# Optimization experiments

Hardware: AMD Instinct MI355X
Metric: run time of the kernel (lower is better)

Reference implementation:

```python
import jax, jax.numpy as jnp
import numpy as np

N_NODES = 100000


def _gcn_norm(edge_index, num_nodes):
    # add self-loops, compute symmetric normalization D^-1/2 (A+I) D^-1/2
    loop = jnp.arange(num_nodes, dtype=edge_index.dtype)
    src = jnp.concatenate([edge_index[0], loop])
    dst = jnp.concatenate([edge_index[1], loop])
    deg = jax.ops.segment_sum(jnp.ones_like(src, dtype=jnp.float32), dst,
                              num_segments=num_nodes)
    dis = jnp.where(deg > 0, jax.lax.rsqrt(jnp.maximum(deg, 1.0)), 0.0)
    norm = dis[src] * dis[dst]  # [E+N]
    return src, dst, norm


def _gcn_conv(x, src, dst, norm, W, b, num_nodes):
    h = x @ W                               # [N, C_out]
    msg = h[src] * norm[:, None]            # gather + scale, [E+N, C_out]
    out = jax.ops.segment_sum(msg, dst, num_segments=num_nodes)
    return out + b


def setup_inputs() -> dict:
    key = jax.random.key(0)
    ks = jax.random.split(key, 8)
    N, E, D = N_NODES, 1600000, 128
    x = jax.random.normal(ks[0], (N, D), dtype=jnp.float32)
    edge_index = jax.random.randint(ks[1], (2, E), 0, N, dtype=jnp.int32)
    s = 1.0 / np.sqrt(D)
    W1 = jax.random.normal(ks[2], (D, D), dtype=jnp.float32) * s
    W2 = jax.random.normal(ks[3], (D, D), dtype=jnp.float32) * s
    W3 = jax.random.normal(ks[4], (D, D), dtype=jnp.float32) * s
    b1 = jnp.zeros((D,), jnp.float32)
    b2 = jnp.zeros((D,), jnp.float32)
    b3 = jnp.zeros((D,), jnp.float32)
    return {"x": x, "edge_index": edge_index, "W1": W1, "b1": b1,
            "W2": W2, "b2": b2, "W3": W3, "b3": b3}


def reference(x, edge_index, W1, b1, W2, b2, W3, b3):
    N = x.shape[0]
    src, dst, norm = _gcn_norm(edge_index, N)
    # layer 1 + relu (dropout p=0 / eval -> identity)
    x = jax.nn.relu(_gcn_conv(x, src, dst, norm, W1, b1, N))
    # layer 2 + relu
    x = jax.nn.relu(_gcn_conv(x, src, dst, norm, W2, b2, N))
    # final layer, no activation
    x = _gcn_conv(x, src, dst, norm, W3, b3, N)
    return x
```

## Files before the change

### kernel.cpp

```cpp
#include <hip/hip_runtime.h>

#define D 128
#define CAP 48
#define PSHIFT 8
#define PNODES 256
#define PMAX 512
#define CAPP 6144
#define EPB 8192

typedef unsigned short u16;
typedef __bf16 bf16_t;
typedef bf16_t bf16x8 __attribute__((ext_vector_type(8)));
typedef float f32x4v __attribute__((ext_vector_type(4)));


__device__ __forceinline__ u16 f2bf(float f) {
    unsigned u = __float_as_uint(f);
    return (u16)((u + 0x7FFFu + ((u >> 16) & 1u)) >> 16);
}

__device__ __forceinline__ float bf2f(u16 h) {
    return __uint_as_float((unsigned)h << 16);
}

__device__ __forceinline__ float4 bf2f4(ushort4 h) {
    float4 f;
    f.x = bf2f(h.x); f.y = bf2f(h.y); f.z = bf2f(h.z); f.w = bf2f(h.w);
    return f;
}

__device__ __forceinline__ void fma4(float4& acc, float xs, const float4& wv) {
    acc.x = fmaf(xs, wv.x, acc.x);
    acc.y = fmaf(xs, wv.y, acc.y);
    acc.z = fmaf(xs, wv.z, acc.z);
    acc.w = fmaf(xs, wv.w, acc.w);
}


__global__ __launch_bounds__(1024) void k_part(const int* __restrict__ src,
                                               const int* __restrict__ dstv,
                                               int* __restrict__ pcur,
                                               int* __restrict__ plist, int E, int P) {
    __shared__ int hist_l[PMAX];
    __shared__ int base_l[PMAX];
    int e0 = blockIdx.x * EPB;
    int e1 = min(e0 + EPB, E);

    for (int i = threadIdx.x; i < P; i += 1024) hist_l[i] = 0;
    __syncthreads();

    for (int e = e0 + threadIdx.x; e < e1; e += 1024)
        atomicAdd(&hist_l[dstv[e] >> PSHIFT], 1);
    __syncthreads();

    for (int i = threadIdx.x; i < P; i += 1024)
        base_l[i] = atomicAdd(&pcur[i], hist_l[i]);
    __syncthreads();

    for (int e = e0 + threadIdx.x; e < e1; e += 1024) {
        int s = src[e], d = dstv[e];
        int p = d >> PSHIFT;
        int pos = atomicAdd(&base_l[p], 1);
        if (pos < CAPP)
            plist[(size_t)p * CAPP + pos] = (s << PSHIFT) | (d & (PNODES - 1));
    }
}


__global__ __launch_bounds__(256) void k_build2(const int* __restrict__ plist,
                                                const int* __restrict__ pcur,
                                                int* __restrict__ cnt,
                                                int* __restrict__ slots, int N) {
    __shared__ int cnt_l[PNODES];
    __shared__ int slots_l[PNODES * CAP];
    int p = blockIdx.x;
    int node0 = p << PSHIFT;
    int nnodes = min(PNODES, N - node0);

    for (int t = threadIdx.x; t < PNODES; t += 256) cnt_l[t] = 0;
    __syncthreads();

    int nE = min(pcur[p], CAPP);
    for (int i = threadIdx.x; i < nE; i += 256) {
        int v = plist[(size_t)p * CAPP + i];
        int ln = v & (PNODES - 1);
        int s = (unsigned)v >> PSHIFT;
        int q = atomicAdd(&cnt_l[ln], 1);
        if (q < CAP) slots_l[ln * CAP + q] = s;
    }
    __syncthreads();

    for (int t = threadIdx.x; t < nnodes; t += 256) cnt[node0 + t] = cnt_l[t];
    int tot = nnodes * CAP;
    int* gs = slots + (size_t)node0 * CAP;
    for (int i = threadIdx.x; i < tot; i += 256) gs[i] = slots_l[i];
}

__global__ void k_dis(const int* __restrict__ cnt, float* __restrict__ dis, int N) {
    int i = blockIdx.x * 256 + threadIdx.x;
    if (i < N) dis[i] = rsqrtf((float)(cnt[i] + 1));
}


__global__ __launch_bounds__(256) void k_gemm(const float* __restrict__ X,
                                              const float* __restrict__ Wg,
                                              u16* __restrict__ H, int nchunks, int N) {
    __shared__ bf16_t sHi[D * D];
    __shared__ bf16_t sLo[D * D];

    for (int i = threadIdx.x; i < D * D; i += 256) {
        int k = i >> 7, n = i & 127;
        float w = Wg[i];
        bf16_t hi = (bf16_t)w;
        bf16_t lo = (bf16_t)(w - (float)hi);
        int idx = (n * D + k) ^ ((n & 7) << 3);
        sHi[idx] = hi;
        sLo[idx] = lo;
    }
    __syncthreads();

    int wv = threadIdx.x >> 6;
    int l  = threadIdx.x & 63;
    int lm = l & 15;
    int g  = l >> 4;

    for (int chunk = blockIdx.x; chunk < nchunks; chunk += gridDim.x) {
        int rowbase = chunk * 128 + wv * 32;
        if (rowbase >= N) continue;

        f32x4v acc[2][8];
#pragma unroll
        for (int rt = 0; rt < 2; ++rt)
#pragma unroll
            for (int c = 0; c < 8; ++c)
#pragma unroll
                for (int r = 0; r < 4; ++r) acc[rt][c][r] = 0.f;

#pragma unroll
        for (int t = 0; t < 4; ++t) {
            bf16x8 ahi[2], alo[2];
#pragma unroll
            for (int rt = 0; rt < 2; ++rt) {
                int row = rowbase + rt * 16 + lm;
                int rc = row < N ? row : N - 1;
                const float4* xp = (const float4*)(X + (size_t)rc * D + t * 32 + g * 8);
                float4 f0 = xp[0];
                float4 f1 = xp[1];
                float fv[8] = {f0.x, f0.y, f0.z, f0.w, f1.x, f1.y, f1.z, f1.w};
#pragma unroll
                for (int i = 0; i < 8; ++i) {
                    bf16_t hb = (bf16_t)fv[i];
                    ahi[rt][i] = hb;
                    alo[rt][i] = (bf16_t)(fv[i] - (float)hb);
                }
            }
#pragma unroll
            for (int c = 0; c < 8; ++c) {
                int idx = ((c * 16 + lm) * D + t * 32 + g * 8) ^ ((lm & 7) << 3);
                bf16x8 bhi = *(const bf16x8*)&sHi[idx];
                bf16x8 blo = *(const bf16x8*)&sLo[idx];
                acc[0][c] = __builtin_amdgcn_mfma_f32_16x16x32_bf16(ahi[0], bhi, acc[0][c], 0, 0, 0);
                acc[0][c] = __builtin_amdgcn_mfma_f32_16x16x32_bf16(ahi[0], blo, acc[0][c], 0, 0, 0);
                acc[0][c] = __builtin_amdgcn_mfma_f32_16x16x32_bf16(alo[0], bhi, acc[0][c], 0, 0, 0);
                acc[1][c] = __builtin_amdgcn_mfma_f32_16x16x32_bf16(ahi[1], bhi, acc[1][c], 0, 0, 0);
                acc[1][c] = __builtin_amdgcn_mfma_f32_16x16x32_bf16(ahi[1], blo, acc[1][c], 0, 0, 0);
                acc[1][c] = __builtin_amdgcn_mfma_f32_16x16x32_bf16(alo[1], bhi, acc[1][c], 0, 0, 0);
            }
        }

#pragma unroll
        for (int rt = 0; rt < 2; ++rt)
#pragma unroll
            for (int r = 0; r < 4; ++r) {
                int row = rowbase + rt * 16 + g * 4 + r;
                if (row >= N) continue;
                u16* hp = H + (size_t)row * D + lm;
#pragma unroll
                for (int c = 0; c < 8; ++c)
                    hp[c * 16] = f2bf(acc[rt][c][r]);
            }
    }
}


__global__ __launch_bounds__(256) void k_agg(const u16* __restrict__ H,
                                             const int* __restrict__ slots,
                                             const int* __restrict__ cnt,
                                             const float* __restrict__ dis,
                                             const float* __restrict__ bias,
                                             float* __restrict__ Y, int N, int relu) {
    int node = (blockIdx.x * 256 + threadIdx.x) >> 5;
    int lane = threadIdx.x & 31;
    if (node >= N) return;

    const ushort4* __restrict__ Hv = (const ushort4*)H;

    float ds = dis[node];
    float4 hv = bf2f4(Hv[(size_t)node * 32 + lane]);
    float wl = ds * ds;
    float4 acc;
    acc.x = wl * hv.x; acc.y = wl * hv.y; acc.z = wl * hv.z; acc.w = wl * hv.w;

    int n = cnt[node];
    if (n > CAP) n = CAP;
    const int* sp = slots + (size_t)node * CAP;

    int e = 0;
    for (; e + 8 <= n; e += 8) {
        int s0 = sp[e + 0], s1 = sp[e + 1], s2 = sp[e + 2], s3 = sp[e + 3];
        int s4 = sp[e + 4], s5 = sp[e + 5], s6 = sp[e + 6], s7 = sp[e + 7];
        ushort4 v0 = Hv[(size_t)s0 * 32 + lane];
        ushort4 v1 = Hv[(size_t)s1 * 32 + lane];
        ushort4 v2 = Hv[(size_t)s2 * 32 + lane];
        ushort4 v3 = Hv[(size_t)s3 * 32 + lane];
        ushort4 v4 = Hv[(size_t)s4 * 32 + lane];
        ushort4 v5 = Hv[(size_t)s5 * 32 + lane];
        ushort4 v6 = Hv[(size_t)s6 * 32 + lane];
        ushort4 v7 = Hv[(size_t)s7 * 32 + lane];
        float w0 = dis[s0] * ds, w1 = dis[s1] * ds, w2 = dis[s2] * ds, w3 = dis[s3] * ds;
        float w4 = dis[s4] * ds, w5 = dis[s5] * ds, w6 = dis[s6] * ds, w7 = dis[s7] * ds;
        fma4(acc, w0, bf2f4(v0));
        fma4(acc, w1, bf2f4(v1));
        fma4(acc, w2, bf2f4(v2));
        fma4(acc, w3, bf2f4(v3));
        fma4(acc, w4, bf2f4(v4));
        fma4(acc, w5, bf2f4(v5));
        fma4(acc, w6, bf2f4(v6));
        fma4(acc, w7, bf2f4(v7));
    }
    for (; e < n; ++e) {
        int s = sp[e];
        ushort4 v = Hv[(size_t)s * 32 + lane];
        fma4(acc, dis[s] * ds, bf2f4(v));
    }

    float4 bv = ((const float4*)bias)[lane];
    acc.x += bv.x; acc.y += bv.y; acc.z += bv.z; acc.w += bv.w;
    if (relu) {
        acc.x = fmaxf(acc.x, 0.f);
        acc.y = fmaxf(acc.y, 0.f);
        acc.z = fmaxf(acc.z, 0.f);
        acc.w = fmaxf(acc.w, 0.f);
    }
    ((float4*)(Y + (size_t)node * D))[lane] = acc;
}


extern "C" void kernel_launch(void* const* d_in, const int* in_sizes, int n_in,
                              void* d_out, int out_size, void* d_ws, size_t ws_size,
                              hipStream_t stream) {
    const float* x  = (const float*)d_in[0];
    const int*   ei = (const int*)d_in[1];
    const float* W1 = (const float*)d_in[2];
    const float* b1 = (const float*)d_in[3];
    const float* W2 = (const float*)d_in[4];
    const float* b2 = (const float*)d_in[5];
    const float* W3 = (const float*)d_in[6];
    const float* b3 = (const float*)d_in[7];
    float* out = (float*)d_out;

    int N = in_sizes[0] / D;
    int E = in_sizes[1] / 2;
    const int* src  = ei;
    const int* dstv = ei + E;
    int P = (N + PNODES - 1) >> PSHIFT;

    char* ws = (char*)d_ws;
    size_t off = 0;
    auto alloc = [&](size_t bytes) -> void* {
        void* p = ws + off;
        off += (bytes + 255) & ~(size_t)255;
        return p;
    };
    u16*   Hbuf  = (u16*)alloc((size_t)N * D * sizeof(u16));
    int*   cnt   = (int*)alloc((size_t)N * sizeof(int));
    int*   slots = (int*)alloc((size_t)N * CAP * sizeof(int));
    float* dis   = (float*)alloc((size_t)N * sizeof(float));
    int*   pcur  = (int*)alloc((size_t)P * sizeof(int));
    int*   plist = (int*)alloc((size_t)P * CAPP * sizeof(int));

    int nchunks = (N + 127) / 128;
    int gemmgrid = 512;
    int aggblocks = (N + 7) / 8;
    int pablocks = (E + EPB - 1) / EPB;

    hipMemsetAsync(pcur, 0, (size_t)P * sizeof(int), stream);
    k_part<<<pablocks, 1024, 0, stream>>>(src, dstv, pcur, plist, E, P);
    k_build2<<<P, 256, 0, stream>>>(plist, pcur, cnt, slots, N);
    k_dis<<<(N + 255) / 256, 256, 0, stream>>>(cnt, dis, N);

    k_gemm<<<gemmgrid, 256, 0, stream>>>(x, W1, Hbuf, nchunks, N);
    k_agg<<<aggblocks, 256, 0, stream>>>(Hbuf, slots, cnt, dis, b1, out, N, 1);

    k_gemm<<<gemmgrid, 256, 0, stream>>>(out, W2, Hbuf, nchunks, N);
    k_agg<<<aggblocks, 256, 0, stream>>>(Hbuf, slots, cnt, dis, b2, out, N, 1);

    k_gemm<<<gemmgrid, 256, 0, stream>>>(out, W3, Hbuf, nchunks, N);
    k_agg<<<aggblocks, 256, 0, stream>>>(Hbuf, slots, cnt, dis, b3, out, N, 0);
}
```

Before: 323.5 us.

## Sort nodes by degree for aggregation and widen gather unrolling

Adds a counting sort of nodes by in-degree (histogram, scan, scatter kernels) and has the aggregation kernel process nodes through this permutation, so half-warps in the same wavefront see similar edge counts and diverge less. It also folds the dis computation into the slot-building kernel, adds 16- and 4-wide unrolled gather loops to raise memory-level parallelism, and sizes the GEMM grid from the chunk count. In exchange there are three extra small kernels, one extra memset, and scattered output writes, since neighbouring threads now write non-adjacent rows.

```diff
diff --git a/kernel.cpp b/kernel.cpp
--- a/kernel.cpp
+++ b/kernel.cpp
@@ -70,7 +70,8 @@
 __global__ __launch_bounds__(256) void k_build2(const int* __restrict__ plist,
                                                 const int* __restrict__ pcur,
                                                 int* __restrict__ cnt,
-                                                int* __restrict__ slots, int N) {
+                                                int* __restrict__ slots,
+                                                float* __restrict__ dis, int N) {
     __shared__ int cnt_l[PNODES];
     __shared__ int slots_l[PNODES * CAP];
     int p = blockIdx.x;
@@ -90,15 +91,53 @@
     }
     __syncthreads();
 
-    for (int t = threadIdx.x; t < nnodes; t += 256) cnt[node0 + t] = cnt_l[t];
+    for (int t = threadIdx.x; t < nnodes; t += 256) {
+        int c = cnt_l[t];
+        cnt[node0 + t] = c;
+        dis[node0 + t] = rsqrtf((float)(c + 1));
+    }
     int tot = nnodes * CAP;
     int* gs = slots + (size_t)node0 * CAP;
     for (int i = threadIdx.x; i < tot; i += 256) gs[i] = slots_l[i];
 }
 
-__global__ void k_dis(const int* __restrict__ cnt, float* __restrict__ dis, int N) {
-    int i = blockIdx.x * 256 + threadIdx.x;
-    if (i < N) dis[i] = rsqrtf((float)(cnt[i] + 1));
+
+__global__ __launch_bounds__(1024) void k_dhist(const int* __restrict__ cnt,
+                                                int* __restrict__ dhist, int N) {
+    __shared__ int h[64];
+    if (threadIdx.x < 64) h[threadIdx.x] = 0;
+    __syncthreads();
+    int i = blockIdx.x * 1024 + threadIdx.x;
+    if (i < N) atomicAdd(&h[min(cnt[i], CAP)], 1);
+    __syncthreads();
+    if (threadIdx.x < 64 && h[threadIdx.x]) atomicAdd(&dhist[threadIdx.x], h[threadIdx.x]);
+}
+
+__global__ void k_dscan(const int* __restrict__ dhist, int* __restrict__ dbase) {
+    if (threadIdx.x == 0) {
+        int acc = 0;
+        for (int b = 0; b < 64; ++b) { dbase[b] = acc; acc += dhist[b]; }
+    }
+}
+
+__global__ __launch_bounds__(1024) void k_dscatter(const int* __restrict__ cnt,
+                                                   int* __restrict__ dbase,
+                                                   int* __restrict__ perm, int N) {
+    __shared__ int h[64], base[64];
+    if (threadIdx.x < 64) h[threadIdx.x] = 0;
+    __syncthreads();
+    int i = blockIdx.x * 1024 + threadIdx.x;
+    int b = 0;
+    if (i < N) { b = min(cnt[i], CAP); atomicAdd(&h[b], 1); }
+    __syncthreads();
+    if (threadIdx.x < 64 && h[threadIdx.x]) base[threadIdx.x] = atomicAdd(&dbase[threadIdx.x], h[threadIdx.x]);
+    __syncthreads();
+    if (threadIdx.x < 64) h[threadIdx.x] = 0;
+    __syncthreads();
+    if (i < N) {
+        int pos = base[b] + atomicAdd(&h[b], 1);
+        perm[pos] = i;
+    }
 }
 
 
@@ -187,11 +226,13 @@
                                              const int* __restrict__ slots,
                                              const int* __restrict__ cnt,
                                              const float* __restrict__ dis,
+                                             const float* __restrict__ perm,
                                              const float* __restrict__ bias,
                                              float* __restrict__ Y, int N, int relu) {
-    int node = (blockIdx.x * 256 + threadIdx.x) >> 5;
+    int hw = (blockIdx.x * 256 + threadIdx.x) >> 5;
     int lane = threadIdx.x & 31;
-    if (node >= N) return;
+    if (hw >= N) return;
+    int node = ((const int*)perm)[hw];
 
     const ushort4* __restrict__ Hv = (const ushort4*)H;
 
@@ -206,27 +247,38 @@
     const int* sp = slots + (size_t)node * CAP;
 
     int e = 0;
+    for (; e + 16 <= n; e += 16) {
+        int ss[16]; ushort4 vv[16]; float ww[16];
+#pragma unroll
+        for (int j = 0; j < 16; ++j) ss[j] = sp[e + j];
+#pragma unroll
+        for (int j = 0; j < 16; ++j) vv[j] = Hv[(size_t)ss[j] * 32 + lane];
+#pragma unroll
+        for (int j = 0; j < 16; ++j) ww[j] = dis[ss[j]] * ds;
+#pragma unroll
+        for (int j = 0; j < 16; ++j) fma4(acc, ww[j], bf2f4(vv[j]));
+    }
     for (; e + 8 <= n; e += 8) {
-        int s0 = sp[e + 0], s1 = sp[e + 1], s2 = sp[e + 2], s3 = sp[e + 3];
-        int s4 = sp[e + 4], s5 = sp[e + 5], s6 = sp[e + 6], s7 = sp[e + 7];
-        ushort4 v0 = Hv[(size_t)s0 * 32 + lane];
-        ushort4 v1 = Hv[(size_t)s1 * 32 + lane];
-        ushort4 v2 = Hv[(size_t)s2 * 32 + lane];
-        ushort4 v3 = Hv[(size_t)s3 * 32 + lane];
-        ushort4 v4 = Hv[(size_t)s4 * 32 + lane];
-        ushort4 v5 = Hv[(size_t)s5 * 32 + lane];
-        ushort4 v6 = Hv[(size_t)s6 * 32 + lane];
-        ushort4 v7 = Hv[(size_t)s7 * 32 + lane];
-        float w0 = dis[s0] * ds, w1 = dis[s1] * ds, w2 = dis[s2] * ds, w3 = dis[s3] * ds;
-        float w4 = dis[s4] * ds, w5 = dis[s5] * ds, w6 = dis[s6] * ds, w7 = dis[s7] * ds;
-        fma4(acc, w0, bf2f4(v0));
-        fma4(acc, w1, bf2f4(v1));
-        fma4(acc, w2, bf2f4(v2));
-        fma4(acc, w3, bf2f4(v3));
-        fma4(acc, w4, bf2f4(v4));
-        fma4(acc, w5, bf2f4(v5));
-        fma4(acc, w6, bf2f4(v6));
-        fma4(acc, w7, bf2f4(v7));
+        int ss[8]; ushort4 vv[8]; float ww[8];
+#pragma unroll
+        for (int j = 0; j < 8; ++j) ss[j] = sp[e + j];
+#pragma unroll
+        for (int j = 0; j < 8; ++j) vv[j] = Hv[(size_t)ss[j] * 32 + lane];
+#pragma unroll
+        for (int j = 0; j < 8; ++j) ww[j] = dis[ss[j]] * ds;
+#pragma unroll
+        for (int j = 0; j < 8; ++j) fma4(acc, ww[j], bf2f4(vv[j]));
+    }
+    for (; e + 4 <= n; e += 4) {
+        int ss[4]; ushort4 vv[4]; float ww[4];
+#pragma unroll
+        for (int j = 0; j < 4; ++j) ss[j] = sp[e + j];
+#pragma unroll
+        for (int j = 0; j < 4; ++j) vv[j] = Hv[(size_t)ss[j] * 32 + lane];
+#pragma unroll
+        for (int j = 0; j < 4; ++j) ww[j] = dis[ss[j]] * ds;
+#pragma unroll
+        for (int j = 0; j < 4; ++j) fma4(acc, ww[j], bf2f4(vv[j]));
     }
     for (; e < n; ++e) {
         int s = sp[e];
@@ -278,23 +330,30 @@
     float* dis   = (float*)alloc((size_t)N * sizeof(float));
     int*   pcur  = (int*)alloc((size_t)P * sizeof(int));
     int*   plist = (int*)alloc((size_t)P * CAPP * sizeof(int));
+    int*   perm  = (int*)alloc((size_t)N * sizeof(int));
+    int*   dhist = (int*)alloc(64 * sizeof(int));
+    int*   dbase = (int*)alloc(64 * sizeof(int));
 
     int nchunks = (N + 127) / 128;
-    int gemmgrid = 512;
+    int gemmgrid = (nchunks + 1) / 2;
     int aggblocks = (N + 7) / 8;
     int pablocks = (E + EPB - 1) / EPB;
+    int nb1k = (N + 1023) / 1024;
 
     hipMemsetAsync(pcur, 0, (size_t)P * sizeof(int), stream);
+    hipMemsetAsync(dhist, 0, 64 * sizeof(int), stream);
     k_part<<<pablocks, 1024, 0, stream>>>(src, dstv, pcur, plist, E, P);
-    k_build2<<<P, 256, 0, stream>>>(plist, pcur, cnt, slots, N);
-    k_dis<<<(N + 255) / 256, 256, 0, stream>>>(cnt, dis, N);
+    k_build2<<<P, 256, 0, stream>>>(plist, pcur, cnt, slots, dis, N);
+    k_dhist<<<nb1k, 1024, 0, stream>>>(cnt, dhist, N);
+    k_dscan<<<1, 64, 0, stream>>>(dhist, dbase);
+    k_dscatter<<<nb1k, 1024, 0, stream>>>(cnt, dbase, perm, N);
 
     k_gemm<<<gemmgrid, 256, 0, stream>>>(x, W1, Hbuf, nchunks, N);
-    k_agg<<<aggblocks, 256, 0, stream>>>(Hbuf, slots, cnt, dis, b1, out, N, 1);
+    k_agg<<<aggblocks, 256, 0, stream>>>(Hbuf, slots, cnt, dis, (const float*)perm, b1, out, N, 1);
 
     k_gemm<<<gemmgrid, 256, 0, stream>>>(out, W2, Hbuf, nchunks, N);
-    k_agg<<<aggblocks, 256, 0, stream>>>(Hbuf, slots, cnt, dis, b2, out, N, 1);
+    k_agg<<<aggblocks, 256, 0, stream>>>(Hbuf, slots, cnt, dis, (const float*)perm, b2, out, N, 1);
 
     k_gemm<<<gemmgrid, 256, 0, stream>>>(out, W3, Hbuf, nchunks, N);
-    k_agg<<<aggblocks, 256, 0, stream>>>(Hbuf, slots, cnt, dis, b3, out, N, 0);
-}
+    k_agg<<<aggblocks, 256, 0, stream>>>(Hbuf, slots, cnt, dis, (const float*)perm, b3, out, N, 0);
+}
```

Result: slower. 339.6 us (+5.0%).
